# Kernel tuning notes

Hardware: AMD Instinct MI355X
Metric: run time of the kernel (lower is better)

Reference implementation:

```python
import jax, jax.numpy as jnp
import numpy as np
from jax import lax

N_NEURONS = 128
BATCH = 2048
SEQ = 128
INFTY = 1e8


def setup_inputs() -> dict:
    key = jax.random.key(0)
    ks = jax.random.split(key, 10)
    n = N_NEURONS
    lim = 1.0 / np.sqrt(n)  # torch LSTMCell default init scale
    return {
        "enc_outputs": jax.random.normal(ks[0], (BATCH, SEQ, n), jnp.float32),
        "h0": jax.random.normal(ks[1], (BATCH, n), jnp.float32),
        "c0": jax.random.normal(ks[2], (BATCH, n), jnp.float32),
        "dec_first_input": jnp.zeros((1, n), jnp.float32),
        "W_ref": jax.random.normal(ks[3], (1, n, n), jnp.float32),
        "W_out": jax.random.normal(ks[4], (n, n), jnp.float32),
        "v": jax.random.normal(ks[5], (n,), jnp.float32),
        "W_ih": jax.random.uniform(ks[6], (4 * n, n), jnp.float32, -lim, lim),
        "W_hh": jax.random.uniform(ks[7], (4 * n, n), jnp.float32, -lim, lim),
        "b_ih": jax.random.uniform(ks[8], (4 * n,), jnp.float32, -lim, lim),
        "b_hh": jax.random.uniform(ks[9], (4 * n,), jnp.float32, -lim, lim),
    }


def _decode(enc_outputs, h0, c0, dec_first_input, W_ref, W_out, v, W_ih, W_hh, b_ih, b_hh):
    B, S, n = enc_outputs.shape
    # step-invariant pointer projection of encoder outputs (the conv1d term)
    enc_term = jnp.einsum("bsn,mn->bsm", enc_outputs, W_ref[0])  # [B,S,n]
    batch_idx = jnp.arange(B)
    keys = jax.random.split(jax.random.key(1234), S)
    inp0 = jnp.broadcast_to(dec_first_input, (B, n))
    mask0 = jnp.zeros((B, S), enc_outputs.dtype)

    def step(carry, key):
        h, c, mask, inp = carry
        # LSTMCell: gate order i, f, g, o (torch convention)
        gates = inp @ W_ih.T + b_ih + h @ W_hh.T + b_hh  # [B,4n]
        i_g, f_g, g_g, o_g = jnp.split(gates, 4, axis=1)
        c = jax.nn.sigmoid(f_g) * c + jax.nn.sigmoid(i_g) * jnp.tanh(g_g)
        h = jax.nn.sigmoid(o_g) * jnp.tanh(c)
        # pointer attention scores
        dec_term = (h @ W_out)[:, None, :]  # [B,1,n]
        scores = jnp.sum(v * jnp.tanh(enc_term + dec_term), axis=-1)  # [B,S]
        masked = scores - INFTY * mask
        loc = jax.random.categorical(key, masked)  # [B] int, non-differentiable sample
        logp = jnp.take_along_axis(jax.nn.log_softmax(masked, axis=1), loc[:, None], axis=1)[:, 0]
        mask = mask.at[batch_idx, loc].set(1.0)
        inp = enc_outputs[batch_idx, loc, :]  # gather next decoder input
        return (h, c, mask, inp), (loc, logp)

    _, (locs, logps) = lax.scan(step, (h0, c0, mask0, inp0), keys)
    locs = locs.T  # [B,S]
    tour = jnp.concatenate([locs, locs[:, :1]], axis=1)  # append first location
    log_prob = jnp.sum(logps, axis=0)  # [B]
    return log_prob, tour


def reference(enc_outputs, h0, c0, dec_first_input, W_ref, W_out, v, W_ih, W_hh, b_ih, b_hh):
    return _decode(enc_outputs, h0, c0, dec_first_input, W_ref, W_out, v, W_ih, W_hh, b_ih, b_hh)
```

## Files before the change

kernel.cpp:

```cpp
#include <hip/hip_runtime.h>
#include <cstdint>
#include <cstddef>

#pragma clang fp contract(off)

#define PRNG_PARTITIONABLE 1

#define INFTY_F 1.0e8f
#define TINY_F 1.17549435e-38f

__device__ __forceinline__ float fdiv_rn(float n, float q) {
  float y0 = __builtin_amdgcn_rcpf(q);
  float y  = fmaf(fmaf(-q, y0, 1.0f), y0, y0);
  float r0 = n * y;
  float e0 = fmaf(-q, r0, n);
  float r1 = fmaf(e0, y, r0);
  float e1 = fmaf(-q, r1, n);
  return fmaf(e1, y, r1);
}

__device__ __forceinline__ void tf2x32(uint32_t k0, uint32_t k1, uint32_t x0, uint32_t x1,
                                       uint32_t& o0, uint32_t& o1) {
  uint32_t ks2 = k0 ^ k1 ^ 0x1BD11BDAu;
  uint32_t v0 = x0 + k0, v1 = x1 + k1;
#define TF_R(r) { v0 += v1; v1 = (v1 << (r)) | (v1 >> (32 - (r))); v1 ^= v0; }
  TF_R(13) TF_R(15) TF_R(26) TF_R(6)
  v0 += k1;  v1 += ks2 + 1u;
  TF_R(17) TF_R(29) TF_R(16) TF_R(24)
  v0 += ks2; v1 += k0 + 2u;
  TF_R(13) TF_R(15) TF_R(26) TF_R(6)
  v0 += k0;  v1 += k1 + 3u;
  TF_R(17) TF_R(29) TF_R(16) TF_R(24)
  v0 += k1;  v1 += ks2 + 4u;
  TF_R(13) TF_R(15) TF_R(26) TF_R(6)
  v0 += ks2; v1 += k0 + 5u;
#undef TF_R
  o0 = v0; o1 = v1;
}

__device__ __forceinline__ uint32_t random_bits32(uint32_t k0, uint32_t k1, uint32_t j) {
#if PRNG_PARTITIONABLE
  uint32_t o0, o1;
  tf2x32(k0, k1, 0u, j, o0, o1);
  return o0 ^ o1;
#else
  uint32_t o0, o1;
  if (j < 131072u) { tf2x32(k0, k1, j, j + 131072u, o0, o1); return o0; }
  else             { tf2x32(k0, k1, j - 131072u, j, o0, o1); return o1; }
#endif
}

__device__ __forceinline__ float xla_tanhf(float x) {
  float xc = fminf(fmaxf(x, -9.0f), 9.0f);
  float x2 = xc * xc;
  float p = -2.76076847742355e-16f;
  p = (p * x2) + 2.00018790482477e-13f;
  p = (p * x2) + -8.60467152213735e-11f;
  p = (p * x2) + 5.12229709037114e-08f;
  p = (p * x2) + 1.48572235717979e-05f;
  p = (p * x2) + 6.37261928875436e-04f;
  p = (p * x2) + 4.89352455891786e-03f;
  float num = xc * p;
  float q = 1.19825839466702e-06f;
  q = (q * x2) + 1.18534705686654e-04f;
  q = (q * x2) + 2.26843463243900e-03f;
  q = (q * x2) + 4.89352518554385e-03f;
  float r = fdiv_rn(num, q);
  return (fabsf(x) < 0.0004f) ? x : r;
}

__device__ __forceinline__ void xla_tanh2(float xa, float xb, float& ra, float& rb) {
  float xca = fminf(fmaxf(xa, -9.0f), 9.0f);
  float xcb = fminf(fmaxf(xb, -9.0f), 9.0f);
  float x2a = xca * xca, x2b = xcb * xcb;
  float pa = -2.76076847742355e-16f, pb = -2.76076847742355e-16f;
  pa = (pa * x2a) + 2.00018790482477e-13f;  pb = (pb * x2b) + 2.00018790482477e-13f;
  pa = (pa * x2a) + -8.60467152213735e-11f; pb = (pb * x2b) + -8.60467152213735e-11f;
  pa = (pa * x2a) + 5.12229709037114e-08f;  pb = (pb * x2b) + 5.12229709037114e-08f;
  pa = (pa * x2a) + 1.48572235717979e-05f;  pb = (pb * x2b) + 1.48572235717979e-05f;
  pa = (pa * x2a) + 6.37261928875436e-04f;  pb = (pb * x2b) + 6.37261928875436e-04f;
  pa = (pa * x2a) + 4.89352455891786e-03f;  pb = (pb * x2b) + 4.89352455891786e-03f;
  float na = xca * pa, nb = xcb * pb;
  float qa = 1.19825839466702e-06f, qb = 1.19825839466702e-06f;
  qa = (qa * x2a) + 1.18534705686654e-04f; qb = (qb * x2b) + 1.18534705686654e-04f;
  qa = (qa * x2a) + 2.26843463243900e-03f; qb = (qb * x2b) + 2.26843463243900e-03f;
  qa = (qa * x2a) + 4.89352518554385e-03f; qb = (qb * x2b) + 4.89352518554385e-03f;
  float da = fdiv_rn(na, qa), db = fdiv_rn(nb, qb);
  ra = (fabsf(xa) < 0.0004f) ? xa : da;
  rb = (fabsf(xb) < 0.0004f) ? xb : db;
}

__device__ __forceinline__ float xla_expf(float x) {
  x = fminf(x, 88.3762626647950f);
  x = fmaxf(x, -88.3762626647949f);
  float m = floorf((x * 1.44269504088896341f) + 0.5f);
  float r = x - (m * 0.693359375f);
  r = r - (m * -2.12194440e-4f);
  float r2 = r * r;
  float y = 1.9875691500E-4f;
  y = (y * r) + 1.3981999507E-3f;
  y = (y * r) + 8.3334519073E-3f;
  y = (y * r) + 4.1665795894E-2f;
  y = (y * r) + 1.6666665459E-1f;
  y = (y * r) + 5.0000001201E-1f;
  y = (y * r2) + r;
  y = y + 1.0f;
  int mi = (int)m;
  float s = __uint_as_float((uint32_t)((mi + 127) << 23));
  return y * s;
}

__device__ __forceinline__ float xla_sigmoidf(float x) {
  return 1.0f / (1.0f + xla_expf(-x));
}

__device__ __forceinline__ float xla_logf(float x) {
  uint32_t b = __float_as_uint(x);
  float e = (float)((int)(b >> 23) - 126);
  float m = __uint_as_float((b & 0x007fffffu) | 0x3f000000u);
  bool mlt = (m < 0.707106781186547524f);
  float tmp = mlt ? m : 0.0f;
  e = e - (mlt ? 1.0f : 0.0f);
  float xx = (m - 1.0f) + tmp;
  float z = xx * xx;
  float y = 7.0376836292E-2f;
  y = (y * xx) + -1.1514610310E-1f;
  y = (y * xx) + 1.1676998740E-1f;
  y = (y * xx) + -1.2420140846E-1f;
  y = (y * xx) + 1.4249322787E-1f;
  y = (y * xx) + -1.6668057665E-1f;
  y = (y * xx) + 2.0000714765E-1f;
  y = (y * xx) + -2.4999993993E-1f;
  y = (y * xx) + 3.3333331174E-1f;
  y = y * xx;
  y = y * z;
  y = y + (e * -2.12194440e-4f);
  y = y - (z * 0.5f);
  float res = xx + y;
  res = res + (e * 0.693359375f);
  return res;
}

__device__ __forceinline__ float gumbel_from_bits(uint32_t bits) {
  float f = __uint_as_float((bits >> 9) | 0x3f800000u) - 1.0f;
  float u = (f * 1.0f) + TINY_F;
  u = fmaxf(TINY_F, u);
  return -xla_logf(-xla_logf(u));
}

__global__ void k_keys(uint32_t* __restrict__ keys) {
  int t = threadIdx.x;
  if (t >= 128) return;
#if PRNG_PARTITIONABLE
  uint32_t o0, o1;
  tf2x32(0u, 1234u, 0u, (uint32_t)t, o0, o1);
  keys[2 * t] = o0; keys[2 * t + 1] = o1;
#else
  uint32_t o0, o1, a, bb;
  if (t < 64) {
    tf2x32(0u, 1234u, (uint32_t)(2 * t),     (uint32_t)(128 + 2 * t), o0, o1); a  = o0;
    tf2x32(0u, 1234u, (uint32_t)(2 * t + 1), (uint32_t)(129 + 2 * t), o0, o1); bb = o0;
  } else {
    tf2x32(0u, 1234u, (uint32_t)(2 * t - 128), (uint32_t)(2 * t),     o0, o1); a  = o1;
    tf2x32(0u, 1234u, (uint32_t)(2 * t - 127), (uint32_t)(2 * t + 1), o0, o1); bb = o1;
  }
  keys[2 * t] = a; keys[2 * t + 1] = bb;
#endif
}

__global__ void k_trans(const float* __restrict__ Wih, const float* __restrict__ Whh,
                        float* __restrict__ WihT, float* __restrict__ WhhT) {
  int idx = blockIdx.x * blockDim.x + threadIdx.x;
  if (idx < 65536) {
    int r = idx >> 7, k = idx & 127;
    WihT[k * 512 + r] = Wih[idx];
    WhhT[k * 512 + r] = Whh[idx];
  }
}

__global__ __launch_bounds__(128) void k_encT(const float* __restrict__ enc,
                                              const float* __restrict__ Wref,
                                              float* __restrict__ encT) {
  __shared__ float el[64 * 132];
  __shared__ float ot[64 * 129];
  int tid = threadIdx.x;
  int b  = blockIdx.x >> 1;
  int sh = blockIdx.x & 1;
  const float* eb = enc + (size_t)b * 16384 + (size_t)sh * 8192;
  for (int i = tid; i < 8192; i += 128) {
    int s = i >> 7, n = i & 127;
    el[s * 132 + n] = eb[i];
  }
  __syncthreads();
  int sl = tid & 63;
  int mh = tid >> 6;
  for (int ml = 0; ml < 64; ++ml) {
    int m = mh * 64 + ml;
    const float4* wr = (const float4*)(Wref + m * 128);
    float acc = 0.0f;
#pragma unroll 8
    for (int q = 0; q < 32; ++q) {
      float4 w4 = wr[q];
      float4 e4 = *(const float4*)&el[sl * 132 + 4 * q];
      acc = fmaf(e4.x, w4.x, acc); acc = fmaf(e4.y, w4.y, acc);
      acc = fmaf(e4.z, w4.z, acc); acc = fmaf(e4.w, w4.w, acc);
    }
    ot[sl * 129 + m] = acc;
  }
  __syncthreads();
  float* op = encT + (size_t)b * 16384 + (size_t)(sh * 64) * 128;
  for (int i = tid; i < 8192; i += 128)
    op[i] = ot[(i >> 7) * 129 + (i & 127)];
}

__global__ __launch_bounds__(512, 4) void k_main(
    const float* __restrict__ enc, const float* __restrict__ h0,
    const float* __restrict__ c0, const float* __restrict__ dec_first,
    const float* __restrict__ W_out, const float* __restrict__ v,
    const float* __restrict__ b_ih, const float* __restrict__ b_hh,
    const float* __restrict__ WihT, const float* __restrict__ WhhT,
    const float* __restrict__ encT, const uint32_t* __restrict__ keys,
    float* __restrict__ out) {
  __shared__ float xI_s[128][8];
  __shared__ float c_s[4][128];
  __shared__ float gates_s[4][512];
  __shared__ float2 vdec2_s[4][128];
  __shared__ float bih_s[512];
  __shared__ float bhh_s[512];
  __shared__ float v_s[128];
  __shared__ uint32_t keys_s[256];
  __shared__ int cu_s[4][128];
  __shared__ int pos_s[4][128];
  __shared__ float red_va[4][2];
  __shared__ int   red_ia[4][2];
  __shared__ float red_mx[4][2];
  __shared__ float red_se[4][2];
  __shared__ float red_msel[4];

  const int tid  = threadIdx.x;
  const int lane = tid & 63;
  const int w    = tid >> 6;
  const int g4   = w >> 1;
  const int half = w & 1;
  const int s4   = half * 64 + lane;
  const int bbase = blockIdx.x * 4;
  const int b4   = bbase + g4;

  bih_s[tid] = b_ih[tid];
  bhh_s[tid] = b_hh[tid];
  if (tid < 256) keys_s[tid] = keys[tid];
  if (tid < 128) v_s[tid] = v[tid];
  {
    int g = tid >> 7, j = tid & 127;
    xI_s[j][g]     = dec_first[j];
    xI_s[j][4 + g] = h0[(size_t)(bbase + g) * 128 + j];
    c_s[g][j] = c0[(size_t)(bbase + g) * 128 + j];
    cu_s[g][j] = j;
    pos_s[g][j] = j;
  }
  float logp_sum = 0.0f;
  float* tour = out + 2048;
  __syncthreads();

  for (int step = 0; step < 128; ++step) {
    {
      const int r = tid;
      float aA0 = 0.0f, aA1 = 0.0f, aA2 = 0.0f, aA3 = 0.0f;
      float aB0 = 0.0f, aB1 = 0.0f, aB2 = 0.0f, aB3 = 0.0f;
      const float* pih = WihT + r;
      const float* phh = WhhT + r;
#pragma unroll 8
      for (int k = 0; k < 128; ++k) {
        float4 xi = *(const float4*)&xI_s[k][0];
        float4 xh = *(const float4*)&xI_s[k][4];
        float wih = pih[k * 512], whh = phh[k * 512];
        aA0 = fmaf(xi.x, wih, aA0);
        aA1 = fmaf(xi.y, wih, aA1);
        aA2 = fmaf(xi.z, wih, aA2);
        aA3 = fmaf(xi.w, wih, aA3);
        aB0 = fmaf(xh.x, whh, aB0);
        aB1 = fmaf(xh.y, whh, aB1);
        aB2 = fmaf(xh.z, whh, aB2);
        aB3 = fmaf(xh.w, whh, aB3);
      }
      float b1 = bih_s[r], b2 = bhh_s[r];
      gates_s[0][r] = (((aA0 + b1) + aB0) + b2);
      gates_s[1][r] = (((aA1 + b1) + aB1) + b2);
      gates_s[2][r] = (((aA2 + b1) + aB2) + b2);
      gates_s[3][r] = (((aA3 + b1) + aB3) + b2);
    }
    __syncthreads();

    {
      int g = tid >> 7, j = tid & 127;
      float gi = gates_s[g][j], gf = gates_s[g][128 + j];
      float gg = gates_s[g][256 + j], go = gates_s[g][384 + j];
      float si = xla_sigmoidf(gi), sf = xla_sigmoidf(gf), so = xla_sigmoidf(go);
      float gt = xla_tanhf(gg);
      float cold = c_s[g][j];
      float cn = (sf * cold) + (si * gt);
      c_s[g][j] = cn;
      xI_s[j][4 + g] = so * xla_tanhf(cn);
    }
    __syncthreads();

    {
      int g = tid >> 7, m = tid & 127;
      float acc = 0.0f;
      const float* wo = W_out + m;
#pragma unroll 8
      for (int k = 0; k < 128; ++k)
        acc = fmaf(xI_s[k][4 + g], wo[k * 128], acc);
      vdec2_s[g][m] = make_float2(v_s[m], acc);
    }
    __syncthreads();

    const int u = 128 - step;
    const bool active = (s4 < u);
    float masked = -INFTY_F;
    float val = -INFTY_F;
    int   ia = 0x7fffffff;
    int   sc = 0;
    if (active) {
      sc = cu_s[g4][s4];
      uint32_t kk0 = keys_s[2 * step], kk1 = keys_s[2 * step + 1];
      uint32_t j0 = (uint32_t)b4 * 128u + (uint32_t)sc;
      float gmb = gumbel_from_bits(random_bits32(kk0, kk1, j0));
      const float* ep = encT + ((size_t)b4 * 128 + (size_t)sc) * 128;
      float acc = 0.0f;
#pragma unroll 8
      for (int m4 = 0; m4 < 32; ++m4) {
        float4 e4 = *(const float4*)&ep[4 * m4];
        float4 vd01 = *(const float4*)&vdec2_s[g4][4 * m4];
        float4 vd23 = *(const float4*)&vdec2_s[g4][4 * m4 + 2];
        float t0, t1, t2, t3;
        xla_tanh2(e4.x + vd01.y, e4.y + vd01.w, t0, t1);
        xla_tanh2(e4.z + vd23.y, e4.w + vd23.w, t2, t3);
        acc = acc + (vd01.x * t0);
        acc = acc + (vd01.z * t1);
        acc = acc + (vd23.x * t2);
        acc = acc + (vd23.z * t3);
      }
      masked = acc;
      val = gmb + masked;
      ia = sc;
    }
    {
      float va = val;
      float mx = masked;
#pragma unroll
      for (int off = 32; off > 0; off >>= 1) {
        float vo = __shfl_xor(va, off, 64);
        int io = __shfl_xor(ia, off, 64);
        if (vo > va || (vo == va && io < ia)) { va = vo; ia = io; }
        mx = fmaxf(mx, __shfl_xor(mx, off, 64));
      }
      float se = expf(masked - mx);
#pragma unroll
      for (int off = 32; off > 0; off >>= 1) se = se + __shfl_xor(se, off, 64);
      if (lane == 0) {
        red_va[g4][half] = va; red_ia[g4][half] = ia;
        red_mx[g4][half] = mx; red_se[g4][half] = se;
      }
      ia = active ? sc : 0x7fffffff;
    }
    __syncthreads();

    float mx2, lse2;
    {
      float vaA = red_va[g4][0], vaB = red_va[g4][1];
      int iaA = red_ia[g4][0], iaB = red_ia[g4][1];
      int loc = (vaB > vaA || (vaB == vaA && iaB < iaA)) ? iaB : iaA;
      if (active && sc == loc) {
        red_msel[g4] = masked;
        tour[(size_t)b4 * 129 + step] = (float)loc;
        if (step == 0) tour[(size_t)b4 * 129 + 128] = (float)loc;
        int p = pos_s[g4][loc];
        int last = cu_s[g4][u - 1];
        cu_s[g4][p] = last;
        pos_s[g4][last] = p;
      }
      const float* er = enc + (size_t)b4 * 16384 + (size_t)loc * 128;
      xI_s[s4][g4] = er[s4];
      float mxA = red_mx[g4][0], mxB = red_mx[g4][1];
      float seA = red_se[g4][0], seB = red_se[g4][1];
      mx2 = fmaxf(mxA, mxB);
      float se2 = seA * expf(mxA - mx2) + seB * expf(mxB - mx2);
      lse2 = logf(se2);
    }
    __syncthreads();
    logp_sum = logp_sum + ((red_msel[g4] - mx2) - lse2);
  }

  if (half == 0 && lane == 0) out[b4] = logp_sum;
}

extern "C" void kernel_launch(void* const* d_in, const int* in_sizes, int n_in,
                              void* d_out, int out_size, void* d_ws, size_t ws_size,
                              hipStream_t stream) {
  (void)in_sizes; (void)n_in; (void)out_size;
  const float* enc       = (const float*)d_in[0];
  const float* h0        = (const float*)d_in[1];
  const float* c0        = (const float*)d_in[2];
  const float* dec_first = (const float*)d_in[3];
  const float* W_ref     = (const float*)d_in[4];
  const float* W_out     = (const float*)d_in[5];
  const float* v         = (const float*)d_in[6];
  const float* W_ih      = (const float*)d_in[7];
  const float* W_hh      = (const float*)d_in[8];
  const float* b_ih      = (const float*)d_in[9];
  const float* b_hh      = (const float*)d_in[10];

  const size_t encT_elems = (size_t)2048 * 16384;
  size_t need = (encT_elems + 65536 + 65536) * sizeof(float) + 256 * sizeof(uint32_t);
  if (ws_size < need) return;

  float* encT = (float*)d_ws;
  float* WihT = encT + encT_elems;
  float* WhhT = WihT + 65536;
  uint32_t* keys = (uint32_t*)(WhhT + 65536);
  float* out = (float*)d_out;

  k_keys<<<dim3(1), dim3(128), 0, stream>>>(keys);
  k_trans<<<dim3(256), dim3(256), 0, stream>>>(W_ih, W_hh, WihT, WhhT);
  k_encT<<<dim3(4096), dim3(128), 0, stream>>>(enc, W_ref, encT);
  k_main<<<dim3(512), dim3(512), 0, stream>>>(enc, h0, c0, dec_first, W_out, v,
                                              b_ih, b_hh, WihT, WhhT, encT, keys, out);
}
```

Before: 6.311 ms.

## Pack active candidates of four batch rows densely across the block's threads

The attention-score stage now maps thread q onto a flattened list of only the still-unvisited candidates of all four batch rows, instead of giving each row a fixed 128 threads. Late in decoding most threads used to sit idle, so compacting the work lets fewer waves do the tanh-heavy scoring. The reduction changes to match: scores are written to shared memory and one wave per row does the argmax, max and sum-exp. This adds a shared-memory round trip and an extra barrier per step, and the softmax and sampling reduction is now serialised onto four waves.

```diff
diff --git a/kernel.cpp b/kernel.cpp
--- a/kernel.cpp
+++ b/kernel.cpp
@@ -231,11 +231,10 @@
   __shared__ uint32_t keys_s[256];
   __shared__ int cu_s[4][128];
   __shared__ int pos_s[4][128];
-  __shared__ float red_va[4][2];
-  __shared__ int   red_ia[4][2];
-  __shared__ float red_mx[4][2];
-  __shared__ float red_se[4][2];
-  __shared__ float red_msel[4];
+  __shared__ float val_s[512];
+  __shared__ float msk_s[512];
+  __shared__ int   sc_s[512];
+  __shared__ int   loc_s[4];
 
   const int tid  = threadIdx.x;
   const int lane = tid & 63;
@@ -316,38 +315,54 @@
     __syncthreads();
 
     const int u = 128 - step;
-    const bool active = (s4 < u);
-    float masked = -INFTY_F;
-    float val = -INFTY_F;
-    int   ia = 0x7fffffff;
-    int   sc = 0;
-    if (active) {
-      sc = cu_s[g4][s4];
-      uint32_t kk0 = keys_s[2 * step], kk1 = keys_s[2 * step + 1];
-      uint32_t j0 = (uint32_t)b4 * 128u + (uint32_t)sc;
-      float gmb = gumbel_from_bits(random_bits32(kk0, kk1, j0));
-      const float* ep = encT + ((size_t)b4 * 128 + (size_t)sc) * 128;
-      float acc = 0.0f;
+    {
+      const int q = tid;
+      float masked = -INFTY_F, val = -INFTY_F;
+      int sc = 0x7fffffff;
+      if (q < 4 * u) {
+        int bq = (q >= u) + (q >= 2 * u) + (q >= 3 * u);
+        int e  = q - bq * u;
+        sc = cu_s[bq][e];
+        const int bb = bbase + bq;
+        uint32_t kk0 = keys_s[2 * step], kk1 = keys_s[2 * step + 1];
+        uint32_t j0 = (uint32_t)bb * 128u + (uint32_t)sc;
+        float gmb = gumbel_from_bits(random_bits32(kk0, kk1, j0));
+        const float* ep = encT + ((size_t)bb * 128 + (size_t)sc) * 128;
+        float acc = 0.0f;
 #pragma unroll 8
-      for (int m4 = 0; m4 < 32; ++m4) {
-        float4 e4 = *(const float4*)&ep[4 * m4];
-        float4 vd01 = *(const float4*)&vdec2_s[g4][4 * m4];
-        float4 vd23 = *(const float4*)&vdec2_s[g4][4 * m4 + 2];
-        float t0, t1, t2, t3;
-        xla_tanh2(e4.x + vd01.y, e4.y + vd01.w, t0, t1);
-        xla_tanh2(e4.z + vd23.y, e4.w + vd23.w, t2, t3);
-        acc = acc + (vd01.x * t0);
-        acc = acc + (vd01.z * t1);
-        acc = acc + (vd23.x * t2);
-        acc = acc + (vd23.z * t3);
+        for (int m4 = 0; m4 < 32; ++m4) {
+          float4 e4 = *(const float4*)&ep[4 * m4];
+          float4 vd01 = *(const float4*)&vdec2_s[bq][4 * m4];
+          float4 vd23 = *(const float4*)&vdec2_s[bq][4 * m4 + 2];
+          float t0, t1, t2, t3;
+          xla_tanh2(e4.x + vd01.y, e4.y + vd01.w, t0, t1);
+          xla_tanh2(e4.z + vd23.y, e4.w + vd23.w, t2, t3);
+          acc = acc + (vd01.x * t0);
+          acc = acc + (vd01.z * t1);
+          acc = acc + (vd23.x * t2);
+          acc = acc + (vd23.z * t3);
+        }
+        masked = acc;
+        val = gmb + masked;
       }
-      masked = acc;
-      val = gmb + masked;
-      ia = sc;
-    }
-    {
-      float va = val;
-      float mx = masked;
+      val_s[q] = val;
+      msk_s[q] = masked;
+      sc_s[q]  = sc;
+    }
+    __syncthreads();
+
+    if (w < 4) {
+      const int g = w;
+      const int base = g * u;
+      float vaA = -INFTY_F, mkA = -INFTY_F;
+      float vaB = -INFTY_F, mkB = -INFTY_F;
+      int iaA = 0x7fffffff, iaB = 0x7fffffff;
+      if (lane < u)      { vaA = val_s[base + lane];      iaA = sc_s[base + lane];      mkA = msk_s[base + lane]; }
+      if (lane + 64 < u) { vaB = val_s[base + lane + 64]; iaB = sc_s[base + lane + 64]; mkB = msk_s[base + lane + 64]; }
+      float va = vaA; int ia = iaA;
+      if (vaB > va || (vaB == va && iaB < ia)) { va = vaB; ia = iaB; }
+      float mx = fmaxf(mkA, mkB);
+      float se = 0.0f;
 #pragma unroll
       for (int off = 32; off > 0; off >>= 1) {
         float vo = __shfl_xor(va, off, 64);
@@ -355,44 +370,35 @@
         if (vo > va || (vo == va && io < ia)) { va = vo; ia = io; }
         mx = fmaxf(mx, __shfl_xor(mx, off, 64));
       }
-      float se = expf(masked - mx);
+      if (lane < u)      se = se + expf(mkA - mx);
+      if (lane + 64 < u) se = se + expf(mkB - mx);
 #pragma unroll
       for (int off = 32; off > 0; off >>= 1) se = se + __shfl_xor(se, off, 64);
+      const int loc = ia;
+      int p = pos_s[g][loc];
+      float msel = msk_s[base + p];
       if (lane == 0) {
-        red_va[g4][half] = va; red_ia[g4][half] = ia;
-        red_mx[g4][half] = mx; red_se[g4][half] = se;
+        loc_s[g] = loc;
+        tour[(size_t)(bbase + g) * 129 + step] = (float)loc;
+        if (step == 0) tour[(size_t)(bbase + g) * 129 + 128] = (float)loc;
+        int last = cu_s[g][u - 1];
+        cu_s[g][p] = last;
+        pos_s[g][last] = p;
       }
-      ia = active ? sc : 0x7fffffff;
-    }
-    __syncthreads();
-
-    float mx2, lse2;
+      float lse = logf(se);
+      logp_sum = logp_sum + ((msel - mx) - lse);
+    }
+    __syncthreads();
+
     {
-      float vaA = red_va[g4][0], vaB = red_va[g4][1];
-      int iaA = red_ia[g4][0], iaB = red_ia[g4][1];
-      int loc = (vaB > vaA || (vaB == vaA && iaB < iaA)) ? iaB : iaA;
-      if (active && sc == loc) {
-        red_msel[g4] = masked;
-        tour[(size_t)b4 * 129 + step] = (float)loc;
-        if (step == 0) tour[(size_t)b4 * 129 + 128] = (float)loc;
-        int p = pos_s[g4][loc];
-        int last = cu_s[g4][u - 1];
-        cu_s[g4][p] = last;
-        pos_s[g4][last] = p;
-      }
+      const int loc = loc_s[g4];
       const float* er = enc + (size_t)b4 * 16384 + (size_t)loc * 128;
       xI_s[s4][g4] = er[s4];
-      float mxA = red_mx[g4][0], mxB = red_mx[g4][1];
-      float seA = red_se[g4][0], seB = red_se[g4][1];
-      mx2 = fmaxf(mxA, mxB);
-      float se2 = seA * expf(mxA - mx2) + seB * expf(mxB - mx2);
-      lse2 = logf(se2);
-    }
-    __syncthreads();
-    logp_sum = logp_sum + ((red_msel[g4] - mx2) - lse2);
-  }
-
-  if (half == 0 && lane == 0) out[b4] = logp_sum;
+    }
+    __syncthreads();
+  }
+
+  if (w < 4 && lane == 0) out[bbase + w] = logp_sum;
 }
 
 extern "C" void kernel_launch(void* const* d_in, const int* in_sizes, int n_in,
```

After: 5.762 ms. 8.7% less time.
